# Performance work log

Hardware: AMD Instinct MI355X
Metric: run time of the kernel (lower is better)

Reference implementation:

```python
import jax, jax.numpy as jnp
import numpy as np

# dims
B, NN, D, HD, L, H, S, FIN = 2048, 64, 128, 128, 4, 8, 8, 16
N = B * NN              # total nodes = 131072
EPG = 8 * NN            # edges per graph (avg degree 8)
E = B * EPG             # total edges = 1048576
A = S * (S - 1)         # num_actions per head = 56


def setup_inputs() -> dict:
    key = jax.random.key(0)
    ks = jax.random.split(key, 16)
    def nrm(k, shape, scale=0.05):
        return jax.random.normal(k, shape, jnp.float32) * scale
    x = jax.random.normal(ks[0], (N, FIN), jnp.float32)
    # per-graph random edges (src/dst local in [0, NN), offset by graph id)
    off = jnp.repeat(jnp.arange(B, dtype=jnp.int32) * NN, EPG)
    src = jax.random.randint(ks[1], (E,), 0, NN, jnp.int32) + off
    dst = jax.random.randint(ks[2], (E,), 0, NN, jnp.int32) + off
    edge_index = jnp.stack([src, dst])
    batch = (jnp.arange(N, dtype=jnp.int32) // NN)
    subsets = jnp.arange(H * S, dtype=jnp.int32).reshape(H, S)
    return dict(
        x=x, edge_index=edge_index, batch=batch, subsets=subsets,
        W_in=nrm(ks[3], (FIN, D)), b_in=jnp.zeros(D, jnp.float32),
        W_self=nrm(ks[4], (L, D, D)), W_nbr=nrm(ks[5], (L, D, D)),
        b_enc=jnp.zeros((L, D), jnp.float32),
        ext_W=nrm(ks[6], (H, 2 * D, HD)), ext_b=jnp.zeros((H, HD), jnp.float32),
        ln_g=jnp.ones((H, HD), jnp.float32), ln_b=jnp.zeros((H, HD), jnp.float32),
        hub_W=nrm(ks[7], (HD, HD)), hub_b=jnp.zeros(HD, jnp.float32),
        pol_W1=nrm(ks[8], (H, 2 * HD, HD)), pol_b1=jnp.zeros((H, HD), jnp.float32),
        pol_W2=nrm(ks[9], (H, HD, A)), pol_b2=jnp.zeros((H, A), jnp.float32),
        val_W1=nrm(ks[10], (D, D)), val_b1=jnp.zeros(D, jnp.float32),
        val_W2=nrm(ks[11], (D, 1)), val_b2=jnp.zeros(1, jnp.float32),
    )


def _forward(floats, edge_index, batch, subsets):
    (x, W_in, b_in, W_self, W_nbr, b_enc, ext_W, ext_b, ln_g, ln_b,
     hub_W, hub_b, pol_W1, pol_b1, pol_W2, pol_b2,
     val_W1, val_b1, val_W2, val_b2) = floats
    src, dst = edge_index[0], edge_index[1]
    # --- GraphEncoder: input proj + L layers of mean-aggregate message passing ---
    deg = jnp.maximum(
        jax.ops.segment_sum(jnp.ones(src.shape[0], x.dtype), dst, num_segments=N), 1.0
    )[:, None]
    h = jax.nn.relu(x @ W_in + b_in)                      # [N, D]
    for l in range(L):
        agg = jax.ops.segment_sum(h[src], dst, num_segments=N) / deg
        h = jax.nn.relu(h @ W_self[l] + agg @ W_nbr[l] + b_enc[l])
    # --- batched per-graph / per-head subset pooling (replaces python loop) ---
    he = h.reshape(B, NN, D)                              # graphs are contiguous in `batch`
    sub = he[:, subsets]                                  # [B, H, S, D]
    pooled = jnp.concatenate([sub.mean(2), sub.max(2)], axis=-1)   # [B, H, 2D]
    z = jnp.einsum('bhf,hfd->bhd', pooled, ext_W) + ext_b
    mu = z.mean(-1, keepdims=True)
    var = z.var(-1, keepdims=True)
    head_emb = jax.nn.relu((z - mu) / jnp.sqrt(var + 1e-5) * ln_g + ln_b)  # [B, H, HD]
    # --- CommunicationHub: shared global context from mean over heads ---
    ctx = jax.nn.relu(head_emb.mean(1) @ hub_W + hub_b)   # [B, HD]
    # --- PolicyHeads: per-head MLP on concat(head_emb, context) ---
    pc = jnp.concatenate(
        [head_emb, jnp.broadcast_to(ctx[:, None, :], head_emb.shape)], axis=-1)
    hh = jax.nn.relu(jnp.einsum('bhf,hfd->bhd', pc, pol_W1) + pol_b1)
    logits = jnp.einsum('bhd,hda->bha', hh, pol_W2) + pol_b2       # [B, H, A]
    # --- ValueHead: per-graph mean pool -> MLP -> tanh ---
    gm = he.mean(1)                                        # segment mean (equal-size graphs)
    v = jnp.tanh(jax.nn.relu(gm @ val_W1 + val_b1) @ val_W2 + val_b2)  # [B, 1]
    return logits, v


def reference(x, edge_index, batch, subsets, W_in, b_in, W_self, W_nbr, b_enc,
              ext_W, ext_b, ln_g, ln_b, hub_W, hub_b, pol_W1, pol_b1, pol_W2,
              pol_b2, val_W1, val_b1, val_W2, val_b2):
    floats = (x, W_in, b_in, W_self, W_nbr, b_enc, ext_W, ext_b, ln_g, ln_b,
              hub_W, hub_b, pol_W1, pol_b1, pol_W2, pol_b2,
              val_W1, val_b1, val_W2, val_b2)
    return _forward(floats, edge_index, batch, subsets)
```

## Files before the change

kernel.cpp:

```cpp
#include <hip/hip_runtime.h>

#define E_TOT 1048576
#define LOGITS 917504

typedef short bf16x8 __attribute__((ext_vector_type(8)));
typedef float f32x4 __attribute__((ext_vector_type(4)));
typedef unsigned short u16;
typedef unsigned int u32;

#define DEV static __device__ __forceinline__

DEV u16 f2bf(float f){ u32 u = __float_as_uint(f); return (u16)((u + 0x7fffu + ((u>>16)&1u))>>16); }
DEV u32 pack2(float a, float b){ return (u32)f2bf(a) | ((u32)f2bf(b)<<16); }
DEV float bf2f(u16 h){ return __uint_as_float(((u32)h)<<16); }
DEV void unpack8(uint4 u, float* f){
  f[0]=__uint_as_float(u.x<<16); f[1]=__uint_as_float(u.x&0xffff0000u);
  f[2]=__uint_as_float(u.y<<16); f[3]=__uint_as_float(u.y&0xffff0000u);
  f[4]=__uint_as_float(u.z<<16); f[5]=__uint_as_float(u.z&0xffff0000u);
  f[6]=__uint_as_float(u.w<<16); f[7]=__uint_as_float(u.w&0xffff0000u);
}
DEV uint4 pack8(const float* f){
  uint4 u; u.x=pack2(f[0],f[1]); u.y=pack2(f[2],f[3]); u.z=pack2(f[4],f[5]); u.w=pack2(f[6],f[7]); return u;
}

#define GNN_E   0
#define EXT_E   131072
#define POL1_E  393216
#define POL2_E  655360
#define HUB_E   720896
#define VW1T_E  737280
#define POOL_E  753664
#define CTX_E   4947968

__global__ __launch_bounds__(256) void pack_w(
    const float* __restrict__ Wself, const float* __restrict__ Wnbr,
    const float* __restrict__ extW,  const float* __restrict__ polW1,
    const float* __restrict__ polW2, const float* __restrict__ hubW,
    const float* __restrict__ valW1, const float* __restrict__ W_in,
    u16* __restrict__ ws)
{
  int idx = (blockIdx.x*256 + threadIdx.x)<<3;
  float v[8];
  if (idx < 131072){
    int l = idx>>15, r = idx&32767;
    int m = (r>>14)&1, r2 = r&16383;
    int kb=(r2>>12)&3, ct=(r2>>9)&7, lane=(r2>>3)&63;
    int k0 = kb*32 + ((lane>>4)<<3), n = (ct<<4)+(lane&15);
    const float* W = m? Wnbr : Wself;
    #pragma unroll
    for (int j=0;j<8;j++) v[j]=W[(l<<14)+((k0+j)<<7)+n];
    *(uint4*)&ws[GNN_E+idx]=pack8(v);
  } else if (idx < 655360){
    int i = idx - 131072;
    int isPol = (i >= 262144); if (isPol) i -= 262144;
    int h = i>>15, r = i&32767;
    int kb=(r>>12)&7, ct=(r>>9)&7, lane=(r>>3)&63;
    int k0 = kb*32 + ((lane>>4)<<3), n = (ct<<4)+(lane&15);
    const float* W = isPol? polW1 : extW;
    #pragma unroll
    for (int j=0;j<8;j++) v[j]=W[(h<<15)+((k0+j)<<7)+n];
    *(uint4*)&ws[(isPol?POL1_E:EXT_E)+i]=pack8(v);
  } else if (idx < 720896){
    int i = idx - 655360;
    int h = i>>13, r = i&8191;
    int kb=(r>>11)&3, ct=(r>>9)&3, lane=(r>>3)&63;
    int k0=kb*32+((lane>>4)<<3), n=(ct<<4)+(lane&15);
    #pragma unroll
    for (int j=0;j<8;j++) v[j]=(n<56)? polW2[h*7168+(k0+j)*56+n] : 0.0f;
    *(uint4*)&ws[POL2_E+i]=pack8(v);
  } else if (idx < 737280){
    int i = idx-720896;
    int kb=(i>>12)&3, ct=(i>>9)&7, lane=(i>>3)&63;
    int k0=kb*32+((lane>>4)<<3), n=(ct<<4)+(lane&15);
    #pragma unroll
    for (int j=0;j<8;j++) v[j]=hubW[((k0+j)<<7)+n];
    *(uint4*)&ws[HUB_E+i]=pack8(v);
  } else if (idx < 753664){
    int i = idx-737280;
    int c = i>>7, k0 = i&127;
    #pragma unroll
    for (int j=0;j<8;j++) v[j]=valW1[((k0+j)<<7)+c];
    *(uint4*)&ws[VW1T_E+i]=pack8(v);
  } else if (idx < 757760){
    int i = idx-753664;
    int ct=(i>>9)&7, lane=(i>>3)&63;
    int k0=((lane>>4)<<3), n=(ct<<4)+(lane&15);
    #pragma unroll
    for (int j=0;j<8;j++) v[j]=(k0+j<16)? W_in[((k0+j)<<7)+n] : 0.0f;
    *(uint4*)&ws[CTX_E+i]=pack8(v);
  }
}

DEV void epi_write(u16* h_bf, u16* ht, f32x4 (&acc)[4][2], float b0, float b1,
                   int wv, int r15, int kh)
{
  float bias[2] = {b0, b1};
  #pragma unroll
  for (int rt=0;rt<4;rt++){
    int sch = (rt<<1)+(kh>>1);
    int r0  = (rt<<4)+(kh<<2);
    #pragma unroll
    for (int cc=0;cc<2;cc++){
      int col=(wv<<5)+(cc<<4)+r15;
      float v0=fmaxf(acc[rt][cc][0]+bias[cc],0.0f);
      float v1=fmaxf(acc[rt][cc][1]+bias[cc],0.0f);
      float v2=fmaxf(acc[rt][cc][2]+bias[cc],0.0f);
      float v3=fmaxf(acc[rt][cc][3]+bias[cc],0.0f);
      int chc=(col>>3);
      h_bf[((r0+0)<<7)+(((chc^((r0+0)&7))<<3)|(col&7))]=f2bf(v0);
      h_bf[((r0+1)<<7)+(((chc^((r0+1)&7))<<3)|(col&7))]=f2bf(v1);
      h_bf[((r0+2)<<7)+(((chc^((r0+2)&7))<<3)|(col&7))]=f2bf(v2);
      h_bf[((r0+3)<<7)+(((chc^((r0+3)&7))<<3)|(col&7))]=f2bf(v3);
      uint2 w; w.x=pack2(v0,v1); w.y=pack2(v2,v3);
      *(uint2*)&ht[(col<<6)+(((sch^(col&7))<<3)|((kh&1)<<2))]=w;
    }
  }
}

__global__ __launch_bounds__(256,3) void gnn_kernel(
  const float* __restrict__ x, const int* __restrict__ ei,
  const int* __restrict__ subsets, const float* __restrict__ b_in,
  const float* __restrict__ b_enc, const float* __restrict__ val_b1,
  const float* __restrict__ val_W2, const float* __restrict__ val_b2,
  const u16* __restrict__ packGNN, const u16* __restrict__ packWIN,
  const u16* __restrict__ valW1T,
  u16* __restrict__ pooled, float* __restrict__ out)
{
  __shared__ __align__(16) u16 h_bf[8192];
  __shared__ __align__(16) u16 ht[8192];
  __shared__ __align__(16) u16 agg_bf[8192];
  __shared__ float deg_inv[64];
  __shared__ int subs_s[64];
  __shared__ float gmbuf[128];
  __shared__ float redbuf[4];

  int t=threadIdx.x, b=blockIdx.x;
  int lane=t&63, wv=t>>6, r15=lane&15, kh=lane>>4, ctb=wv<<1;
  u32* cnt=(u32*)ht;
  f32x4 zero4={0.0f,0.0f,0.0f,0.0f};

  int e0=(b<<9)+(t<<1);
  int2 sp=*(const int2*)&ei[e0];
  int2 dp=*(const int2*)&ei[E_TOT+e0];
  int s0=sp.x&63, s1=sp.y&63, d0=dp.x&63, d1=dp.y&63;
  if (t<64) subs_s[t]=subsets[t];
  for (int i=t;i<1024;i+=256) ((uint4*)cnt)[i]=make_uint4(0,0,0,0);
  __syncthreads();
  atomicAdd(&cnt[(d0<<6)+((((s0>>3)^(d0&7))<<3)|(s0&7))],1u);
  atomicAdd(&cnt[(d1<<6)+((((s1>>3)^(d1&7))<<3)|(s1&7))],1u);
  __syncthreads();
  if (t<64){
    u32 s=0;
    for (int k2=0;k2<16;k2++){ uint4 vv=((uint4*)cnt)[(t<<4)+k2]; s+=vv.x+vv.y+vv.z+vv.w; }
    deg_inv[t]=1.0f/(float)(s>0u?s:1u);
  }
  __syncthreads();

  bf16x8 adjf[4][2];
  #pragma unroll
  for (int ct=0;ct<4;ct++){
    int dst=(ct<<4)+r15; float di=deg_inv[dst];
    #pragma unroll
    for (int kb=0;kb<2;kb++){
      int cb=(kb<<2)+kh;
      const u32* p=&cnt[(dst<<6)+((cb^(dst&7))<<3)];
      uint4 lo=*(const uint4*)p, hi=*(const uint4*)(p+4);
      uint4 pk;
      pk.x=pack2((float)lo.x*di,(float)lo.y*di);
      pk.y=pack2((float)lo.z*di,(float)lo.w*di);
      pk.z=pack2((float)hi.x*di,(float)hi.y*di);
      pk.w=pack2((float)hi.z*di,(float)hi.w*di);
      adjf[ct][kb]=*(bf16x8*)&pk;
    }
  }

  u16* xb=agg_bf;
  { int row=t>>2, c0=(t&3)<<3;
    float v[8];
    if (c0<16){
      const float* xg=x+(b<<10)+(row<<4)+c0;
      #pragma unroll
      for (int j=0;j<8;j++) v[j]=xg[j];
    } else {
      #pragma unroll
      for (int j=0;j<8;j++) v[j]=0.0f;
    }
    *(uint4*)&xb[(row<<5)+((((c0>>3)^(row&3))<<3))]=pack8(v);
  }
  __syncthreads();

  {
    bf16x8 bw0=*(const bf16x8*)&packWIN[(ctb<<9)+(lane<<3)];
    bf16x8 bw1=*(const bf16x8*)&packWIN[((ctb+1)<<9)+(lane<<3)];
    f32x4 acc[4][2];
    #pragma unroll
    for (int rt=0;rt<4;rt++){ acc[rt][0]=zero4; acc[rt][1]=zero4; }
    #pragma unroll
    for (int rt=0;rt<4;rt++){
      int row=(rt<<4)+r15;
      bf16x8 af=*(const bf16x8*)&xb[(row<<5)+((kh^(row&3))<<3)];
      acc[rt][0]=__builtin_amdgcn_mfma_f32_16x16x32_bf16(af,bw0,acc[rt][0],0,0,0);
      acc[rt][1]=__builtin_amdgcn_mfma_f32_16x16x32_bf16(af,bw1,acc[rt][1],0,0,0);
    }
    float bi0=b_in[(wv<<5)+r15], bi1=b_in[(wv<<5)+16+r15];
    epi_write(h_bf,ht,acc,bi0,bi1,wv,r15,kh);
  }
  __syncthreads();

  #pragma unroll 1
  for (int l=0;l<4;l++){
    const u16* pl = packGNN + (l<<15);
    f32x4 a2[2][4];
    #pragma unroll
    for (int rt=0;rt<2;rt++){ a2[rt][0]=zero4; a2[rt][1]=zero4; a2[rt][2]=zero4; a2[rt][3]=zero4; }
    #pragma unroll
    for (int kb=0;kb<2;kb++){
      #pragma unroll
      for (int rt=0;rt<2;rt++){
        int dim=((ctb+rt)<<4)+r15;
        bf16x8 af=*(const bf16x8*)&ht[(dim<<6)+((((kb<<2)+kh)^(dim&7))<<3)];
        #pragma unroll
        for (int ct=0;ct<4;ct++)
          a2[rt][ct]=__builtin_amdgcn_mfma_f32_16x16x32_bf16(af,adjf[ct][kb],a2[rt][ct],0,0,0);
      }
    }
    #pragma unroll
    for (int rt=0;rt<2;rt++){
      int dch=((ctb+rt)<<1)+(kh>>1);
      #pragma unroll
      for (int ct=0;ct<4;ct++){
        int node=(ct<<4)+r15;
        uint2 w; w.x=pack2(a2[rt][ct][0],a2[rt][ct][1]); w.y=pack2(a2[rt][ct][2],a2[rt][ct][3]);
        *(uint2*)&agg_bf[(node<<7)+(((dch^(node&7))<<3)|((kh&1)<<2))]=w;
      }
    }
    __syncthreads();
    f32x4 acc[4][2];
    #pragma unroll
    for (int rt=0;rt<4;rt++){ acc[rt][0]=zero4; acc[rt][1]=zero4; }
    #pragma unroll 2
    for (int kb=0;kb<4;kb++){
      int ch=(kb<<2)+kh;
      bf16x8 bs0=*(const bf16x8*)&pl[(kb<<12)+(ctb<<9)+(lane<<3)];
      bf16x8 bs1=*(const bf16x8*)&pl[(kb<<12)+((ctb+1)<<9)+(lane<<3)];
      bf16x8 bn0=*(const bf16x8*)&pl[16384+(kb<<12)+(ctb<<9)+(lane<<3)];
      bf16x8 bn1=*(const bf16x8*)&pl[16384+(kb<<12)+((ctb+1)<<9)+(lane<<3)];
      #pragma unroll
      for (int rt=0;rt<4;rt++){
        int row=(rt<<4)+r15;
        bf16x8 af=*(const bf16x8*)&h_bf[(row<<7)+((ch^(row&7))<<3)];
        acc[rt][0]=__builtin_amdgcn_mfma_f32_16x16x32_bf16(af,bs0,acc[rt][0],0,0,0);
        acc[rt][1]=__builtin_amdgcn_mfma_f32_16x16x32_bf16(af,bs1,acc[rt][1],0,0,0);
      }
      #pragma unroll
      for (int rt=0;rt<4;rt++){
        int row=(rt<<4)+r15;
        bf16x8 ag=*(const bf16x8*)&agg_bf[(row<<7)+((ch^(row&7))<<3)];
        acc[rt][0]=__builtin_amdgcn_mfma_f32_16x16x32_bf16(ag,bn0,acc[rt][0],0,0,0);
        acc[rt][1]=__builtin_amdgcn_mfma_f32_16x16x32_bf16(ag,bn1,acc[rt][1],0,0,0);
      }
    }
    float be0=b_enc[(l<<7)+(wv<<5)+r15], be1=b_enc[(l<<7)+(wv<<5)+16+r15];
    __syncthreads();
    epi_write(h_bf,ht,acc,be0,be1,wv,r15,kh);
    __syncthreads();
  }

  {
    int hd=t>>5, q=t&31, cb=q<<2;
    float ms[4]={0,0,0,0}, mx[4]={-3e38f,-3e38f,-3e38f,-3e38f};
    int ch=cb>>3;
    #pragma unroll
    for (int s=0;s<8;s++){
      int row=subs_s[(hd<<3)+s]; int sw=row&7;
      uint2 u=*(const uint2*)&h_bf[(row<<7)+(((ch^sw)<<3)|(cb&7))];
      float f0=__uint_as_float(u.x<<16), f1=__uint_as_float(u.x&0xffff0000u);
      float f2=__uint_as_float(u.y<<16), f3=__uint_as_float(u.y&0xffff0000u);
      ms[0]+=f0; ms[1]+=f1; ms[2]+=f2; ms[3]+=f3;
      mx[0]=fmaxf(mx[0],f0); mx[1]=fmaxf(mx[1],f1);
      mx[2]=fmaxf(mx[2],f2); mx[3]=fmaxf(mx[3],f3);
    }
    int base=(((b<<3)+hd)<<8);
    uint2 um,ux;
    um.x=pack2(ms[0]*0.125f,ms[1]*0.125f); um.y=pack2(ms[2]*0.125f,ms[3]*0.125f);
    ux.x=pack2(mx[0],mx[1]);               ux.y=pack2(mx[2],mx[3]);
    *(uint2*)&pooled[base+cb]    =um;
    *(uint2*)&pooled[base+128+cb]=ux;
  }

  float gsum=0.0f;
  if (t<128){
    #pragma unroll
    for (int c=0;c<8;c++){
      uint4 u=*(const uint4*)&ht[(t<<6)+(c<<3)];
      float f[8]; unpack8(u,f);
      gsum+=f[0]+f[1]+f[2]+f[3]+f[4]+f[5]+f[6]+f[7];
    }
  }
  __syncthreads();
  if (t<128) gmbuf[t]=gsum*0.015625f;
  __syncthreads();
  if (t<128){
    float acc=val_b1[t];
    const uint4* wr=(const uint4*)&valW1T[t<<7];
    #pragma unroll
    for (int c=0;c<16;c++){
      uint4 u=wr[c]; float f[8]; unpack8(u,f);
      const float* gp=&gmbuf[c<<3];
      #pragma unroll
      for (int j=0;j<8;j++) acc=fmaf(gp[j],f[j],acc);
    }
    float contrib=fmaxf(acc,0.0f)*val_W2[t];
    #pragma unroll
    for (int d=1;d<64;d<<=1) contrib+=__shfl_xor(contrib,d);
    if (lane==0) redbuf[wv]=contrib;
  }
  __syncthreads();
  if (t==0) out[LOGITS+b]=tanhf(redbuf[0]+redbuf[1]+val_b2[0]);
}

__global__ __launch_bounds__(256) void heads_kernel(
  const u16* __restrict__ pooled, const u16* __restrict__ packExt,
  const float* __restrict__ ext_b, const float* __restrict__ ln_g,
  const float* __restrict__ ln_b, const u16* __restrict__ packHub,
  const float* __restrict__ hub_b, const u16* __restrict__ packPol1,
  const u16* __restrict__ packPol2, const float* __restrict__ pol_b1,
  const float* __restrict__ pol_b2, float* __restrict__ out)
{
  __shared__ __align__(16) u16 A_lds[2048];
  __shared__ float zf[8*132];
  __shared__ __align__(16) u16 he[8192];
  __shared__ __align__(16) u16 ctx_l[1024];
  __shared__ __align__(16) u16 m_lds[1024];
  __shared__ __align__(16) u16 hh[1024];
  int t=threadIdx.x, gb=blockIdx.x;
  int lane=t&63, wv=t>>6, r15=lane&15, kh=lane>>4, ctb=wv<<1;
  int ar=r15&7;
  f32x4 zero4={0.0f,0.0f,0.0f,0.0f};

  for (int hd=0; hd<8; ++hd){
    { int row=t>>5, ch=t&31;
      uint4 u=*(const uint4*)&pooled[(((((gb<<3)+row)<<3)+hd)<<8)+(ch<<3)];
      *(uint4*)&A_lds[(row<<8)+((ch^(row&7))<<3)]=u;
    }
    __syncthreads();
    const u16* pw=packExt+(hd<<15);
    f32x4 acc[2]={zero4,zero4};
    #pragma unroll
    for (int kb=0;kb<8;kb++){
      int ch=(kb<<2)+kh;
      bf16x8 a=*(const bf16x8*)&A_lds[(ar<<8)+((ch^ar)<<3)];
      bf16x8 b0=*(const bf16x8*)&pw[(kb<<12)+(ctb<<9)+(lane<<3)];
      bf16x8 b1=*(const bf16x8*)&pw[(kb<<12)+((ctb+1)<<9)+(lane<<3)];
      acc[0]=__builtin_amdgcn_mfma_f32_16x16x32_bf16(a,b0,acc[0],0,0,0);
      acc[1]=__builtin_amdgcn_mfma_f32_16x16x32_bf16(a,b1,acc[1],0,0,0);
    }
    if (kh<2){
      float eb[2]={ext_b[(hd<<7)+(wv<<5)+r15], ext_b[(hd<<7)+(wv<<5)+16+r15]};
      #pragma unroll
      for (int cc=0;cc<2;cc++){
        int col=(wv<<5)+(cc<<4)+r15;
        #pragma unroll
        for (int i=0;i<4;i++) zf[((kh<<2)+i)*132+col]=acc[cc][i]+eb[cc];
      }
    }
    __syncthreads();
    if (t<128){
      int row=t>>4, q=t&15;
      const float* zr=&zf[row*132+(q<<3)];
      float s=0,ss=0;
      #pragma unroll
      for (int i=0;i<8;i++){ float v=zr[i]; s+=v; ss+=v*v; }
      s+=__shfl_xor(s,1); ss+=__shfl_xor(ss,1);
      s+=__shfl_xor(s,2); ss+=__shfl_xor(ss,2);
      s+=__shfl_xor(s,4); ss+=__shfl_xor(ss,4);
      s+=__shfl_xor(s,8); ss+=__shfl_xor(ss,8);
      float mu=s*0.0078125f, var=ss*0.0078125f-mu*mu, rstd=rsqrtf(var+1e-5f);
      const float* g=&ln_g[(hd<<7)+(q<<3)];
      const float* bb=&ln_b[(hd<<7)+(q<<3)];
      float e[8];
      #pragma unroll
      for (int i=0;i<8;i++) e[i]=fmaxf((zr[i]-mu)*rstd*g[i]+bb[i],0.0f);
      int r=(row<<3)+hd;
      *(uint4*)&he[(r<<7)+((q^hd)<<3)]=pack8(e);
    }
    __syncthreads();
  }

  if (t<128){
    int row=t>>4, ch=t&15;
    float a8[8]={0,0,0,0,0,0,0,0};
    #pragma unroll
    for (int h=0;h<8;h++){
      uint4 u=*(const uint4*)&he[(((row<<3)+h)<<7)+((ch^h)<<3)];
      float f[8]; unpack8(u,f);
      #pragma unroll
      for (int k=0;k<8;k++) a8[k]+=f[k];
    }
    #pragma unroll
    for (int k=0;k<8;k++) a8[k]*=0.125f;
    *(uint4*)&m_lds[(row<<7)+((ch^(row&7))<<3)]=pack8(a8);
  }
  __syncthreads();
  {
    f32x4 acc[2]={zero4,zero4};
    #pragma unroll
    for (int kb=0;kb<4;kb++){
      int ch=(kb<<2)+kh;
      bf16x8 a=*(const bf16x8*)&m_lds[(ar<<7)+((ch^ar)<<3)];
      bf16x8 b0=*(const bf16x8*)&packHub[(kb<<12)+(ctb<<9)+(lane<<3)];
      bf16x8 b1=*(const bf16x8*)&packHub[(kb<<12)+((ctb+1)<<9)+(lane<<3)];
      acc[0]=__builtin_amdgcn_mfma_f32_16x16x32_bf16(a,b0,acc[0],0,0,0);
      acc[1]=__builtin_amdgcn_mfma_f32_16x16x32_bf16(a,b1,acc[1],0,0,0);
    }
    if (kh<2){
      float hb[2]={hub_b[(wv<<5)+r15], hub_b[(wv<<5)+16+r15]};
      #pragma unroll
      for (int cc=0;cc<2;cc++){
        int col=(wv<<5)+(cc<<4)+r15;
        #pragma unroll
        for (int i=0;i<4;i++){
          int row=(kh<<2)+i;
          ctx_l[(row<<7)+((((col>>3)^(row&7))<<3)|(col&7))]=f2bf(fmaxf(acc[cc][i]+hb[cc],0.0f));
        }
      }
    }
  }
  __syncthreads();

  for (int hd=0; hd<8; ++hd){
    { int row=t>>5, ch=t&31;
      uint4 u;
      if (ch<16){ int r=(row<<3)+hd; u=*(const uint4*)&he[(r<<7)+((ch^hd)<<3)]; }
      else        u=*(const uint4*)&ctx_l[(row<<7)+(((ch-16)^(row&7))<<3)];
      *(uint4*)&A_lds[(row<<8)+((ch^(row&7))<<3)]=u;
    }
    __syncthreads();
    const u16* pw=packPol1+(hd<<15);
    f32x4 acc[2]={zero4,zero4};
    #pragma unroll
    for (int kb=0;kb<8;kb++){
      int ch=(kb<<2)+kh;
      bf16x8 a=*(const bf16x8*)&A_lds[(ar<<8)+((ch^ar)<<3)];
      bf16x8 b0=*(const bf16x8*)&pw[(kb<<12)+(ctb<<9)+(lane<<3)];
      bf16x8 b1=*(const bf16x8*)&pw[(kb<<12)+((ctb+1)<<9)+(lane<<3)];
      acc[0]=__builtin_amdgcn_mfma_f32_16x16x32_bf16(a,b0,acc[0],0,0,0);
      acc[1]=__builtin_amdgcn_mfma_f32_16x16x32_bf16(a,b1,acc[1],0,0,0);
    }
    if (kh<2){
      float pb[2]={pol_b1[(hd<<7)+(wv<<5)+r15], pol_b1[(hd<<7)+(wv<<5)+16+r15]};
      #pragma unroll
      for (int cc=0;cc<2;cc++){
        int col=(wv<<5)+(cc<<4)+r15;
        #pragma unroll
        for (int i=0;i<4;i++){
          int row=(kh<<2)+i;
          float v=fmaxf(acc[cc][i]+pb[cc],0.0f);
          hh[(row<<7)+((((col>>3)^(row&7))<<3)|(col&7))]=f2bf(v);
        }
      }
    }
    __syncthreads();
    const u16* p2=packPol2+(hd<<13);
    f32x4 a2=zero4;
    #pragma unroll
    for (int kb=0;kb<4;kb++){
      int ch=(kb<<2)+kh;
      bf16x8 a=*(const bf16x8*)&hh[(ar<<7)+((ch^ar)<<3)];
      bf16x8 b2=*(const bf16x8*)&p2[(kb<<11)+(wv<<9)+(lane<<3)];
      a2=__builtin_amdgcn_mfma_f32_16x16x32_bf16(a,b2,a2,0,0,0);
    }
    int col=(wv<<4)+r15;
    if (col<56 && kh<2){
      float pb2=pol_b2[hd*56+col];
      #pragma unroll
      for (int i=0;i<4;i++){
        int row=(kh<<2)+i;
        out[(((((gb<<3)+row)<<3)+hd)*56)+col]=a2[i]+pb2;
      }
    }
    __syncthreads();
  }
}

extern "C" void kernel_launch(void* const* d_in, const int* in_sizes, int n_in,
                              void* d_out, int out_size, void* d_ws, size_t ws_size,
                              hipStream_t stream)
{
  const float* x     =(const float*)d_in[0];
  const int*   ei    =(const int*)  d_in[1];
  const int*   subs  =(const int*)  d_in[3];
  const float* W_in  =(const float*)d_in[4];
  const float* b_in  =(const float*)d_in[5];
  const float* W_self=(const float*)d_in[6];
  const float* W_nbr =(const float*)d_in[7];
  const float* b_enc =(const float*)d_in[8];
  const float* extW  =(const float*)d_in[9];
  const float* ext_b =(const float*)d_in[10];
  const float* ln_g  =(const float*)d_in[11];
  const float* ln_b  =(const float*)d_in[12];
  const float* hubW  =(const float*)d_in[13];
  const float* hub_b =(const float*)d_in[14];
  const float* polW1 =(const float*)d_in[15];
  const float* pol_b1=(const float*)d_in[16];
  const float* polW2 =(const float*)d_in[17];
  const float* pol_b2=(const float*)d_in[18];
  const float* valW1 =(const float*)d_in[19];
  const float* val_b1=(const float*)d_in[20];
  const float* valW2 =(const float*)d_in[21];
  const float* val_b2=(const float*)d_in[22];
  float* out=(float*)d_out;
  u16* ws=(u16*)d_ws;

  pack_w<<<370,256,0,stream>>>(W_self,W_nbr,extW,polW1,polW2,hubW,valW1,W_in,ws);
  gnn_kernel<<<2048,256,0,stream>>>(x,ei,subs,b_in,b_enc,val_b1,valW2,val_b2,
      ws+GNN_E, ws+CTX_E, ws+VW1T_E, ws+POOL_E, out);
  heads_kernel<<<256,256,0,stream>>>(ws+POOL_E, ws+EXT_E, ext_b, ln_g, ln_b,
      ws+HUB_E, hub_b, ws+POL1_E, ws+POL2_E, pol_b1, pol_b2, out);
}
```

Before: 217.4 us.

## Split GNN block work across 8 waves instead of 4

Launches the GNN kernel with 512 threads per block and gives each wave a 16-column slice instead of 32, halving per-wave accumulators and MFMA work. Each thread now handles one edge for the adjacency build, and the x load and pooling stages are gated to the first 256 threads. The aim is more waves in flight per CU to hide LDS and MFMA latency, with launch bounds raised to match. The cost is more barrier participants and idle threads in the gated stages, and the higher wave count may be limited by LDS per block.

```diff
diff --git a/kernel.cpp b/kernel.cpp
--- a/kernel.cpp
+++ b/kernel.cpp
@@ -91,33 +91,29 @@
   }
 }
 
-DEV void epi_write(u16* h_bf, u16* ht, f32x4 (&acc)[4][2], float b0, float b1,
-                   int wv, int r15, int kh)
+DEV void epi_write8(u16* h_bf, u16* ht, f32x4 (&acc)[4], float bias,
+                    int wv, int r15, int kh)
 {
-  float bias[2] = {b0, b1};
+  int col=(wv<<4)+r15;
+  int chc=col>>3;
   #pragma unroll
   for (int rt=0;rt<4;rt++){
     int sch = (rt<<1)+(kh>>1);
     int r0  = (rt<<4)+(kh<<2);
-    #pragma unroll
-    for (int cc=0;cc<2;cc++){
-      int col=(wv<<5)+(cc<<4)+r15;
-      float v0=fmaxf(acc[rt][cc][0]+bias[cc],0.0f);
-      float v1=fmaxf(acc[rt][cc][1]+bias[cc],0.0f);
-      float v2=fmaxf(acc[rt][cc][2]+bias[cc],0.0f);
-      float v3=fmaxf(acc[rt][cc][3]+bias[cc],0.0f);
-      int chc=(col>>3);
-      h_bf[((r0+0)<<7)+(((chc^((r0+0)&7))<<3)|(col&7))]=f2bf(v0);
-      h_bf[((r0+1)<<7)+(((chc^((r0+1)&7))<<3)|(col&7))]=f2bf(v1);
-      h_bf[((r0+2)<<7)+(((chc^((r0+2)&7))<<3)|(col&7))]=f2bf(v2);
-      h_bf[((r0+3)<<7)+(((chc^((r0+3)&7))<<3)|(col&7))]=f2bf(v3);
-      uint2 w; w.x=pack2(v0,v1); w.y=pack2(v2,v3);
-      *(uint2*)&ht[(col<<6)+(((sch^(col&7))<<3)|((kh&1)<<2))]=w;
-    }
-  }
-}
-
-__global__ __launch_bounds__(256,3) void gnn_kernel(
+    float v0=fmaxf(acc[rt][0]+bias,0.0f);
+    float v1=fmaxf(acc[rt][1]+bias,0.0f);
+    float v2=fmaxf(acc[rt][2]+bias,0.0f);
+    float v3=fmaxf(acc[rt][3]+bias,0.0f);
+    h_bf[((r0+0)<<7)+(((chc^((r0+0)&7))<<3)|(col&7))]=f2bf(v0);
+    h_bf[((r0+1)<<7)+(((chc^((r0+1)&7))<<3)|(col&7))]=f2bf(v1);
+    h_bf[((r0+2)<<7)+(((chc^((r0+2)&7))<<3)|(col&7))]=f2bf(v2);
+    h_bf[((r0+3)<<7)+(((chc^((r0+3)&7))<<3)|(col&7))]=f2bf(v3);
+    uint2 w; w.x=pack2(v0,v1); w.y=pack2(v2,v3);
+    *(uint2*)&ht[(col<<6)+(((sch^(col&7))<<3)|((kh&1)<<2))]=w;
+  }
+}
+
+__global__ __launch_bounds__(512,6) void gnn_kernel(
   const float* __restrict__ x, const int* __restrict__ ei,
   const int* __restrict__ subsets, const float* __restrict__ b_in,
   const float* __restrict__ b_enc, const float* __restrict__ val_b1,
@@ -135,19 +131,16 @@
   __shared__ float redbuf[4];
 
   int t=threadIdx.x, b=blockIdx.x;
-  int lane=t&63, wv=t>>6, r15=lane&15, kh=lane>>4, ctb=wv<<1;
+  int lane=t&63, wv=t>>6, r15=lane&15, kh=lane>>4;
   u32* cnt=(u32*)ht;
   f32x4 zero4={0.0f,0.0f,0.0f,0.0f};
 
-  int e0=(b<<9)+(t<<1);
-  int2 sp=*(const int2*)&ei[e0];
-  int2 dp=*(const int2*)&ei[E_TOT+e0];
-  int s0=sp.x&63, s1=sp.y&63, d0=dp.x&63, d1=dp.y&63;
+  int e0=(b<<9)+t;
+  int s0=ei[e0]&63, d0=ei[E_TOT+e0]&63;
   if (t<64) subs_s[t]=subsets[t];
-  for (int i=t;i<1024;i+=256) ((uint4*)cnt)[i]=make_uint4(0,0,0,0);
+  for (int i=t;i<1024;i+=512) ((uint4*)cnt)[i]=make_uint4(0,0,0,0);
   __syncthreads();
   atomicAdd(&cnt[(d0<<6)+((((s0>>3)^(d0&7))<<3)|(s0&7))],1u);
-  atomicAdd(&cnt[(d1<<6)+((((s1>>3)^(d1&7))<<3)|(s1&7))],1u);
   __syncthreads();
   if (t<64){
     u32 s=0;
@@ -175,7 +168,8 @@
   }
 
   u16* xb=agg_bf;
-  { int row=t>>2, c0=(t&3)<<3;
+  if (t<256){
+    int row=t>>2, c0=(t&3)<<3;
     float v[8];
     if (c0<16){
       const float* xg=x+(b<<10)+(row<<4)+c0;
@@ -190,83 +184,73 @@
   __syncthreads();
 
   {
-    bf16x8 bw0=*(const bf16x8*)&packWIN[(ctb<<9)+(lane<<3)];
-    bf16x8 bw1=*(const bf16x8*)&packWIN[((ctb+1)<<9)+(lane<<3)];
-    f32x4 acc[4][2];
-    #pragma unroll
-    for (int rt=0;rt<4;rt++){ acc[rt][0]=zero4; acc[rt][1]=zero4; }
+    bf16x8 bw=*(const bf16x8*)&packWIN[(wv<<9)+(lane<<3)];
+    f32x4 acc[4];
+    #pragma unroll
+    for (int rt=0;rt<4;rt++) acc[rt]=zero4;
     #pragma unroll
     for (int rt=0;rt<4;rt++){
       int row=(rt<<4)+r15;
       bf16x8 af=*(const bf16x8*)&xb[(row<<5)+((kh^(row&3))<<3)];
-      acc[rt][0]=__builtin_amdgcn_mfma_f32_16x16x32_bf16(af,bw0,acc[rt][0],0,0,0);
-      acc[rt][1]=__builtin_amdgcn_mfma_f32_16x16x32_bf16(af,bw1,acc[rt][1],0,0,0);
-    }
-    float bi0=b_in[(wv<<5)+r15], bi1=b_in[(wv<<5)+16+r15];
-    epi_write(h_bf,ht,acc,bi0,bi1,wv,r15,kh);
+      acc[rt]=__builtin_amdgcn_mfma_f32_16x16x32_bf16(af,bw,acc[rt],0,0,0);
+    }
+    float bi=b_in[(wv<<4)+r15];
+    epi_write8(h_bf,ht,acc,bi,wv,r15,kh);
   }
   __syncthreads();
 
   #pragma unroll 1
   for (int l=0;l<4;l++){
     const u16* pl = packGNN + (l<<15);
-    f32x4 a2[2][4];
-    #pragma unroll
-    for (int rt=0;rt<2;rt++){ a2[rt][0]=zero4; a2[rt][1]=zero4; a2[rt][2]=zero4; a2[rt][3]=zero4; }
+    f32x4 a2[4];
+    #pragma unroll
+    for (int ct=0;ct<4;ct++) a2[ct]=zero4;
     #pragma unroll
     for (int kb=0;kb<2;kb++){
-      #pragma unroll
-      for (int rt=0;rt<2;rt++){
-        int dim=((ctb+rt)<<4)+r15;
-        bf16x8 af=*(const bf16x8*)&ht[(dim<<6)+((((kb<<2)+kh)^(dim&7))<<3)];
-        #pragma unroll
-        for (int ct=0;ct<4;ct++)
-          a2[rt][ct]=__builtin_amdgcn_mfma_f32_16x16x32_bf16(af,adjf[ct][kb],a2[rt][ct],0,0,0);
-      }
-    }
-    #pragma unroll
-    for (int rt=0;rt<2;rt++){
-      int dch=((ctb+rt)<<1)+(kh>>1);
+      int dim=(wv<<4)+r15;
+      bf16x8 af=*(const bf16x8*)&ht[(dim<<6)+((((kb<<2)+kh)^(dim&7))<<3)];
+      #pragma unroll
+      for (int ct=0;ct<4;ct++)
+        a2[ct]=__builtin_amdgcn_mfma_f32_16x16x32_bf16(af,adjf[ct][kb],a2[ct],0,0,0);
+    }
+    {
+      int dch=(wv<<1)+(kh>>1);
       #pragma unroll
       for (int ct=0;ct<4;ct++){
         int node=(ct<<4)+r15;
-        uint2 w; w.x=pack2(a2[rt][ct][0],a2[rt][ct][1]); w.y=pack2(a2[rt][ct][2],a2[rt][ct][3]);
+        uint2 w; w.x=pack2(a2[ct][0],a2[ct][1]); w.y=pack2(a2[ct][2],a2[ct][3]);
         *(uint2*)&agg_bf[(node<<7)+(((dch^(node&7))<<3)|((kh&1)<<2))]=w;
       }
     }
     __syncthreads();
-    f32x4 acc[4][2];
-    #pragma unroll
-    for (int rt=0;rt<4;rt++){ acc[rt][0]=zero4; acc[rt][1]=zero4; }
+    f32x4 acc[4];
+    #pragma unroll
+    for (int rt=0;rt<4;rt++) acc[rt]=zero4;
     #pragma unroll 2
     for (int kb=0;kb<4;kb++){
       int ch=(kb<<2)+kh;
-      bf16x8 bs0=*(const bf16x8*)&pl[(kb<<12)+(ctb<<9)+(lane<<3)];
-      bf16x8 bs1=*(const bf16x8*)&pl[(kb<<12)+((ctb+1)<<9)+(lane<<3)];
-      bf16x8 bn0=*(const bf16x8*)&pl[16384+(kb<<12)+(ctb<<9)+(lane<<3)];
-      bf16x8 bn1=*(const bf16x8*)&pl[16384+(kb<<12)+((ctb+1)<<9)+(lane<<3)];
+      bf16x8 bs=*(const bf16x8*)&pl[(kb<<12)+(wv<<9)+(lane<<3)];
+      bf16x8 bn=*(const bf16x8*)&pl[16384+(kb<<12)+(wv<<9)+(lane<<3)];
       #pragma unroll
       for (int rt=0;rt<4;rt++){
         int row=(rt<<4)+r15;
         bf16x8 af=*(const bf16x8*)&h_bf[(row<<7)+((ch^(row&7))<<3)];
-        acc[rt][0]=__builtin_amdgcn_mfma_f32_16x16x32_bf16(af,bs0,acc[rt][0],0,0,0);
-        acc[rt][1]=__builtin_amdgcn_mfma_f32_16x16x32_bf16(af,bs1,acc[rt][1],0,0,0);
+        acc[rt]=__builtin_amdgcn_mfma_f32_16x16x32_bf16(af,bs,acc[rt],0,0,0);
       }
       #pragma unroll
       for (int rt=0;rt<4;rt++){
         int row=(rt<<4)+r15;
         bf16x8 ag=*(const bf16x8*)&agg_bf[(row<<7)+((ch^(row&7))<<3)];
-        acc[rt][0]=__builtin_amdgcn_mfma_f32_16x16x32_bf16(ag,bn0,acc[rt][0],0,0,0);
-        acc[rt][1]=__builtin_amdgcn_mfma_f32_16x16x32_bf16(ag,bn1,acc[rt][1],0,0,0);
-      }
-    }
-    float be0=b_enc[(l<<7)+(wv<<5)+r15], be1=b_enc[(l<<7)+(wv<<5)+16+r15];
-    __syncthreads();
-    epi_write(h_bf,ht,acc,be0,be1,wv,r15,kh);
-    __syncthreads();
-  }
-
-  {
+        acc[rt]=__builtin_amdgcn_mfma_f32_16x16x32_bf16(ag,bn,acc[rt],0,0,0);
+      }
+    }
+    float be=b_enc[(l<<7)+(wv<<4)+r15];
+    __syncthreads();
+    epi_write8(h_bf,ht,acc,be,wv,r15,kh);
+    __syncthreads();
+  }
+
+  if (t<256){
     int hd=t>>5, q=t&31, cb=q<<2;
     float ms[4]={0,0,0,0}, mx[4]={-3e38f,-3e38f,-3e38f,-3e38f};
     int ch=cb>>3;
@@ -513,7 +497,7 @@
   u16* ws=(u16*)d_ws;
 
   pack_w<<<370,256,0,stream>>>(W_self,W_nbr,extW,polW1,polW2,hubW,valW1,W_in,ws);
-  gnn_kernel<<<2048,256,0,stream>>>(x,ei,subs,b_in,b_enc,val_b1,valW2,val_b2,
+  gnn_kernel<<<2048,512,0,stream>>>(x,ei,subs,b_in,b_enc,val_b1,valW2,val_b2,
       ws+GNN_E, ws+CTX_E, ws+VW1T_E, ws+POOL_E, out);
   heads_kernel<<<256,256,0,stream>>>(ws+POOL_E, ws+EXT_E, ext_b, ln_g, ln_b,
       ws+HUB_E, hub_b, ws+POL1_E, ws+POL2_E, pol_b1, pol_b2, out);
```

Result: slower. 261.8 us (+20.4%).
